# Kernel tuning notes

Hardware: AMD Instinct MI355X
Metric: run time of the kernel (lower is better)

## Reference

```python
import jax, jax.numpy as jnp
import numpy as np

BLOCK_SIZE = 16
NVFP4_LEVELS = np.array([0.0, 0.5, 1.0, 1.5, 2.0, 3.0, 4.0, 6.0], dtype=np.float32)


def quantize_to_nvfp4(x, block_size=BLOCK_SIZE):
    """NVFP4 fake-quant: per-16-element block, scale = amax/6, round |x| to nearest level."""
    levels = jnp.asarray(NVFP4_LEVELS, dtype=x.dtype)
    orig_shape = x.shape
    xf = x.reshape(-1, block_size)                                   # [nblk, 16]
    amax = jnp.clip(jnp.max(jnp.abs(xf), axis=-1, keepdims=True), 1e-12)
    scale = amax / 6.0                                               # [nblk, 1]
    x_norm = jnp.abs(xf) / scale                                     # in [0, 6]
    idx = jnp.argmin(jnp.abs(x_norm[..., None] - levels), axis=-1)   # nearest level (first on ties, like torch)
    x_q = jnp.sign(xf) * levels[idx] * scale
    return x_q.reshape(orig_shape)


def _magnitude_mask_2_4(w):
    # keep 2 largest-|.| of every group of 4 along in_features (row-wise 2:4)
    out_f, in_f = w.shape
    a = jnp.abs(w).reshape(out_f, in_f // 4, 4)
    thr = jnp.sort(a, axis=-1)[..., 2:3]          # 2nd-largest magnitude in group
    mask = (a >= thr).reshape(out_f, in_f)
    return mask.astype(w.dtype)


def setup_inputs() -> dict:
    key = jax.random.key(0)
    k_x, k_w, k_s, k_a, k_b, k_bias = jax.random.split(key, 6)
    B, S, IN_F, OUT_F, RANK = 2, 2048, 4096, 4096, 32
    x = jax.random.normal(k_x, (B, S, IN_F), dtype=jnp.float32)
    smooth_scale = jax.random.uniform(k_s, (IN_F,), dtype=jnp.float32, minval=0.5, maxval=2.0)
    # realistic calibrated weight: 2:4 magnitude-sparse then NVFP4 fake-quantized
    w = jax.random.normal(k_w, (OUT_F, IN_F), dtype=jnp.float32) * 0.02
    w_sparse = w * _magnitude_mask_2_4(w)
    w_quantized = quantize_to_nvfp4(w_sparse)
    lora_a = jax.random.normal(k_a, (RANK, IN_F), dtype=jnp.float32) * 0.02
    lora_b = jax.random.normal(k_b, (OUT_F, RANK), dtype=jnp.float32) * 0.02
    bias = jax.random.normal(k_bias, (OUT_F,), dtype=jnp.float32)
    return {"x": x, "smooth_scale": smooth_scale, "w_quantized": w_quantized,
            "lora_a": lora_a, "lora_b": lora_b, "bias": bias}


def reference(x, smooth_scale, w_quantized, lora_a, lora_b, bias):
    # x: [B, S, IN], smooth_scale: [IN], w_quantized: [OUT, IN]
    x_smoothed = x * smooth_scale                                    # SmoothQuant activation scaling
    x_q = quantize_to_nvfp4(x_smoothed, BLOCK_SIZE)                  # block fake-quant of activations
    base_out = jnp.einsum('bsi,oi->bso', x_q, w_quantized)           # 2:4-sparse quantized matmul
    svd_out = jnp.einsum('bsr,or->bso',
                         jnp.einsum('bsi,ri->bsr', x_smoothed, lora_a), lora_b)  # low-rank correction
    return base_out + svd_out + bias
```

## Files before the change

kernel.cpp:

```cpp
#include <hip/hip_runtime.h>
#include <hip/hip_bf16.h>
#include <stdint.h>

typedef __attribute__((ext_vector_type(8)))  __bf16 bf16x8;
typedef __attribute__((ext_vector_type(4)))  float  f32x4;
typedef __attribute__((ext_vector_type(16))) float  f32x16;

#define KP 4160

__device__ inline void async_copy16(const void* g, void* l) {
  __builtin_amdgcn_global_load_lds((const __attribute__((address_space(1))) void*)g,
                                   (__attribute__((address_space(3))) void*)l, 16, 0, 0);
}

__global__ __launch_bounds__(256) void fused_quant_lora_kernel(
    const float* __restrict__ x, const float* __restrict__ ss,
    const float* __restrict__ la, __bf16* __restrict__ Ab,
    float* __restrict__ Tp) {
  __shared__ float red[4][16][32];
  int tid  = threadIdx.x;
  int m0   = blockIdx.x << 4;
  int by   = blockIdx.y;

  {
    int row = m0 + (tid >> 4);
    int cb0 = tid & 15;
#pragma unroll
    for (int i = 0; i < 4; i++) {
      int col = (by << 10) + ((cb0 + (i << 4)) << 4);
      const float4* xp = (const float4*)(x + ((size_t)row << 12) + col);
      const float4* sp = (const float4*)(ss + col);
      float xs[16];
#pragma unroll
      for (int j = 0; j < 4; j++) {
        float4 xv = xp[j]; float4 sv = sp[j];
        xs[4*j+0] = xv.x * sv.x; xs[4*j+1] = xv.y * sv.y;
        xs[4*j+2] = xv.z * sv.z; xs[4*j+3] = xv.w * sv.w;
      }
      float amax = 0.f;
#pragma unroll
      for (int j = 0; j < 16; j++) amax = fmaxf(amax, fabsf(xs[j]));
      amax = fmaxf(amax, 1e-12f);
      float scale = amax / 6.0f;
      bf16x8 o0, o1;
#pragma unroll
      for (int j = 0; j < 16; j++) {
        float a  = fabsf(xs[j]);
        float xn = a / scale;
        float bestd = xn;
        float lvl   = 0.f;
        const float L[7] = {0.5f, 1.f, 1.5f, 2.f, 3.f, 4.f, 6.f};
#pragma unroll
        for (int l = 0; l < 7; l++) {
          float d = fabsf(xn - L[l]);
          if (d < bestd) { bestd = d; lvl = L[l]; }
        }
        float mag = lvl * scale;
        float q = (xs[j] > 0.f) ? mag : ((xs[j] < 0.f) ? -mag : 0.f);
        if (j < 8) o0[j] = (__bf16)q; else o1[j-8] = (__bf16)q;
      }
      __bf16* dst = Ab + (size_t)row * KP + col;
      *(bf16x8*)dst = o0;
      *(bf16x8*)(dst + 8) = o1;
    }
  }

  {
    int wave = tid >> 6, lane = tid & 63;
    int lrow = lane & 15, kg = lane >> 4;
    int kbase = (by << 10) + (wave << 8);
    f32x4 acc0 = {0.f,0.f,0.f,0.f}, acc1 = {0.f,0.f,0.f,0.f};
    const float* xrow = x + ((size_t)(m0 + lrow) << 12);
    const float* a0   = la + ((size_t)lrow << 12);
    const float* a1   = a0 + (16 << 12);
#pragma unroll
    for (int k0 = 0; k0 < 256; k0 += 32) {
      int kk = kbase + k0 + (kg << 3);
      float xv[8], sv[8], v0[8], v1[8];
      *(float4*)&xv[0] = *(const float4*)(xrow + kk);
      *(float4*)&xv[4] = *(const float4*)(xrow + kk + 4);
      *(float4*)&sv[0] = *(const float4*)(ss + kk);
      *(float4*)&sv[4] = *(const float4*)(ss + kk + 4);
      *(float4*)&v0[0] = *(const float4*)(a0 + kk);
      *(float4*)&v0[4] = *(const float4*)(a0 + kk + 4);
      *(float4*)&v1[0] = *(const float4*)(a1 + kk);
      *(float4*)&v1[4] = *(const float4*)(a1 + kk + 4);
      bf16x8 af, b0, b1;
#pragma unroll
      for (int j = 0; j < 8; j++) {
        af[j] = (__bf16)(xv[j] * sv[j]);
        b0[j] = (__bf16)v0[j];
        b1[j] = (__bf16)v1[j];
      }
      acc0 = __builtin_amdgcn_mfma_f32_16x16x32_bf16(af, b0, acc0, 0, 0, 0);
      acc1 = __builtin_amdgcn_mfma_f32_16x16x32_bf16(af, b1, acc1, 0, 0, 0);
    }
#pragma unroll
    for (int r = 0; r < 4; r++) {
      red[wave][kg*4 + r][lrow]      = acc0[r];
      red[wave][kg*4 + r][16 + lrow] = acc1[r];
    }
    __syncthreads();
    for (int o = tid; o < 512; o += 256) {
      int rr = o >> 5, cc = o & 31;
      float s = red[0][rr][cc] + red[1][rr][cc] + red[2][rr][cc] + red[3][rr][cc];
      Tp[((size_t)by * 4096 + m0 + rr) * 32 + cc] = s;
    }
  }
}

__global__ __launch_bounds__(256) void wconv_fix_kernel(const float* __restrict__ w,
                                                        const float* __restrict__ lb,
                                                        const float* __restrict__ Tp,
                                                        __bf16* __restrict__ Bb,
                                                        __bf16* __restrict__ Ab) {
  int b = blockIdx.x;
  if (b < 8320) {
    int id  = b * 256 + threadIdx.x;
    int row = id / 520;
    int g   = id - row * 520;
    bf16x8 v;
    if (g < 512) {
      const float4* wp = (const float4*)(w + ((size_t)row << 12) + (g << 3));
      float4 a = wp[0], bb = wp[1];
      v[0]=(__bf16)a.x;  v[1]=(__bf16)a.y;  v[2]=(__bf16)a.z;  v[3]=(__bf16)a.w;
      v[4]=(__bf16)bb.x; v[5]=(__bf16)bb.y; v[6]=(__bf16)bb.z; v[7]=(__bf16)bb.w;
    } else if (g < 516) {
      const float* p = lb + (size_t)row * 32 + ((g - 512) << 3);
#pragma unroll
      for (int j = 0; j < 8; j++) v[j] = (__bf16)p[j];
    } else {
#pragma unroll
      for (int j = 0; j < 8; j++) v[j] = (__bf16)0.f;
    }
    *(bf16x8*)(Bb + (size_t)row * KP + ((size_t)g << 3)) = v;
  } else {
    int id  = (b - 8320) * 256 + threadIdx.x;
    int row = id >> 5, cc = id & 31;
    float s = 0.f;
#pragma unroll
    for (int kc = 0; kc < 4; kc++)
      s += Tp[((size_t)kc * 4096 + row) * 32 + cc];
    __bf16* dst = Ab + (size_t)row * KP + 4096;
    dst[cc]      = (__bf16)s;
    dst[32 + cc] = (__bf16)0.f;
  }
}

__global__ __launch_bounds__(256) void gemm_kernel(const __bf16* __restrict__ A,
                                                   const __bf16* __restrict__ B,
                                                   const float* __restrict__ bias,
                                                   float* __restrict__ C) {
  __shared__ __bf16 As[128 * 64];
  __shared__ __bf16 Bs[128 * 64];
  int tid  = threadIdx.x;
  int wave = tid >> 6, lane = tid & 63;
  int bm = blockIdx.x >> 5, bn = blockIdx.x & 31;
  size_t m0 = (size_t)bm << 7, n0 = (size_t)bn << 7;
  int wm = wave >> 1, wn = wave & 1;
  int ln31 = lane & 31, kgrp = lane >> 5;
  int srow = lane >> 3;
  int sk   = ((lane & 7) ^ srow) << 3;
  int swz  = (ln31 & 7) << 4;
  f32x16 acc[2][2];
#pragma unroll
  for (int r = 0; r < 2; r++)
#pragma unroll
    for (int c = 0; c < 2; c++)
#pragma unroll
      for (int q = 0; q < 16; q++) acc[r][c][q] = 0.f;

  for (int k = 0; k < KP; k += 64) {
#pragma unroll
    for (int i = 0; i < 4; i++) {
      int chunk = (wave << 2) + i;
      int row   = (chunk << 3) + srow;
      async_copy16(A + (m0 + row) * (size_t)KP + k + sk, (void*)(As + chunk * 512));
      async_copy16(B + (n0 + row) * (size_t)KP + k + sk, (void*)(Bs + chunk * 512));
    }
    __syncthreads();
#pragma unroll
    for (int t = 0; t < 4; t++) {
      int kx = ((t << 5) + (kgrp << 4)) ^ swz;
      bf16x8 af[2], bfr[2];
#pragma unroll
      for (int h = 0; h < 2; h++) {
        int arow = (wm << 6) + (h << 5) + ln31;
        af[h]  = *(const bf16x8*)((const char*)As + arow * 128 + kx);
        int brow = (wn << 6) + (h << 5) + ln31;
        bfr[h] = *(const bf16x8*)((const char*)Bs + brow * 128 + kx);
      }
#pragma unroll
      for (int r = 0; r < 2; r++)
#pragma unroll
        for (int c = 0; c < 2; c++)
          acc[r][c] = __builtin_amdgcn_mfma_f32_32x32x16_bf16(af[r], bfr[c], acc[r][c], 0, 0, 0);
    }
    __syncthreads();
  }
#pragma unroll
  for (int c = 0; c < 2; c++) {
    int col = (int)n0 + (wn << 6) + (c << 5) + ln31;
    float bv = bias[col];
#pragma unroll
    for (int r = 0; r < 2; r++) {
      size_t rowb = m0 + (wm << 6) + (r << 5) + (kgrp << 2);
#pragma unroll
      for (int q = 0; q < 16; q++) {
        size_t row = rowb + (q & 3) + ((q >> 2) << 3);
        C[row * 4096 + col] = acc[r][c][q] + bv;
      }
    }
  }
}

extern "C" void kernel_launch(void* const* d_in, const int* in_sizes, int n_in,
                              void* d_out, int out_size, void* d_ws, size_t ws_size,
                              hipStream_t stream) {
  const float* x    = (const float*)d_in[0];
  const float* ss   = (const float*)d_in[1];
  const float* w    = (const float*)d_in[2];
  const float* la   = (const float*)d_in[3];
  const float* lb   = (const float*)d_in[4];
  const float* bias = (const float*)d_in[5];
  float* out = (float*)d_out;

  __bf16* Ab = (__bf16*)d_ws;
  __bf16* Bb = Ab + (size_t)4096 * KP;
  float* Tp = out;

  fused_quant_lora_kernel<<<dim3(256, 4), 256, 0, stream>>>(x, ss, la, Ab, Tp);
  wconv_fix_kernel<<<8832, 256, 0, stream>>>(w, lb, Tp, Bb, Ab);
  gemm_kernel<<<1024, 256, 0, stream>>>(Ab, Bb, bias, out);
}
```

Baseline: 348.3 us.

## Rewrite GEMM as 256x256 tiled, double-buffered, barrier-scheduled 8-wave kernel

Replaces the 128x128, single-buffered GEMM with a 256x256 tile per 512-thread block. It double-buffers 128 KB of dynamic LDS, interleaves async global-to-LDS copies with MFMA phases, and uses s_setprio and explicit vmcnt waits to overlap loads with compute. K padding grows to 4224 so K is a multiple of 128 for the two-stage pipeline, with extra zero fill. A block-index swizzle improves L2 locality. This targets the low arithmetic intensity and exposed load latency of the old GEMM, at the cost of heavy register and LDS use and only 256 blocks.

```diff
diff --git a/kernel.cpp b/kernel.cpp
--- a/kernel.cpp
+++ b/kernel.cpp
@@ -4,9 +4,8 @@
 
 typedef __attribute__((ext_vector_type(8)))  __bf16 bf16x8;
 typedef __attribute__((ext_vector_type(4)))  float  f32x4;
-typedef __attribute__((ext_vector_type(16))) float  f32x16;
-
-#define KP 4160
+
+#define KP 4224
 
 __device__ inline void async_copy16(const void* g, void* l) {
   __builtin_amdgcn_global_load_lds((const __attribute__((address_space(1))) void*)g,
@@ -115,10 +114,10 @@
                                                         __bf16* __restrict__ Bb,
                                                         __bf16* __restrict__ Ab) {
   int b = blockIdx.x;
-  if (b < 8320) {
+  if (b < 8448) {
     int id  = b * 256 + threadIdx.x;
-    int row = id / 520;
-    int g   = id - row * 520;
+    int row = id / 528;
+    int g   = id - row * 528;
     bf16x8 v;
     if (g < 512) {
       const float4* wp = (const float4*)(w + ((size_t)row << 12) + (g << 3));
@@ -135,7 +134,7 @@
     }
     *(bf16x8*)(Bb + (size_t)row * KP + ((size_t)g << 3)) = v;
   } else {
-    int id  = (b - 8320) * 256 + threadIdx.x;
+    int id  = (b - 8448) * 256 + threadIdx.x;
     int row = id >> 5, cc = id & 31;
     float s = 0.f;
 #pragma unroll
@@ -144,72 +143,129 @@
     __bf16* dst = Ab + (size_t)row * KP + 4096;
     dst[cc]      = (__bf16)s;
     dst[32 + cc] = (__bf16)0.f;
-  }
-}
-
-__global__ __launch_bounds__(256) void gemm_kernel(const __bf16* __restrict__ A,
-                                                   const __bf16* __restrict__ B,
-                                                   const float* __restrict__ bias,
-                                                   float* __restrict__ C) {
-  __shared__ __bf16 As[128 * 64];
-  __shared__ __bf16 Bs[128 * 64];
-  int tid  = threadIdx.x;
-  int wave = tid >> 6, lane = tid & 63;
-  int bm = blockIdx.x >> 5, bn = blockIdx.x & 31;
-  size_t m0 = (size_t)bm << 7, n0 = (size_t)bn << 7;
-  int wm = wave >> 1, wn = wave & 1;
-  int ln31 = lane & 31, kgrp = lane >> 5;
-  int srow = lane >> 3;
-  int sk   = ((lane & 7) ^ srow) << 3;
-  int swz  = (ln31 & 7) << 4;
-  f32x16 acc[2][2];
-#pragma unroll
-  for (int r = 0; r < 2; r++)
-#pragma unroll
-    for (int c = 0; c < 2; c++)
-#pragma unroll
-      for (int q = 0; q < 16; q++) acc[r][c][q] = 0.f;
-
-  for (int k = 0; k < KP; k += 64) {
-#pragma unroll
-    for (int i = 0; i < 4; i++) {
-      int chunk = (wave << 2) + i;
-      int row   = (chunk << 3) + srow;
-      async_copy16(A + (m0 + row) * (size_t)KP + k + sk, (void*)(As + chunk * 512));
-      async_copy16(B + (n0 + row) * (size_t)KP + k + sk, (void*)(Bs + chunk * 512));
-    }
-    __syncthreads();
-#pragma unroll
-    for (int t = 0; t < 4; t++) {
-      int kx = ((t << 5) + (kgrp << 4)) ^ swz;
-      bf16x8 af[2], bfr[2];
-#pragma unroll
-      for (int h = 0; h < 2; h++) {
-        int arow = (wm << 6) + (h << 5) + ln31;
-        af[h]  = *(const bf16x8*)((const char*)As + arow * 128 + kx);
-        int brow = (wn << 6) + (h << 5) + ln31;
-        bfr[h] = *(const bf16x8*)((const char*)Bs + brow * 128 + kx);
-      }
-#pragma unroll
-      for (int r = 0; r < 2; r++)
-#pragma unroll
-        for (int c = 0; c < 2; c++)
-          acc[r][c] = __builtin_amdgcn_mfma_f32_32x32x16_bf16(af[r], bfr[c], acc[r][c], 0, 0, 0);
-    }
-    __syncthreads();
-  }
-#pragma unroll
-  for (int c = 0; c < 2; c++) {
-    int col = (int)n0 + (wn << 6) + (c << 5) + ln31;
-    float bv = bias[col];
-#pragma unroll
-    for (int r = 0; r < 2; r++) {
-      size_t rowb = m0 + (wm << 6) + (r << 5) + (kgrp << 2);
-#pragma unroll
-      for (int q = 0; q < 16; q++) {
-        size_t row = rowb + (q & 3) + ((q >> 2) << 3);
-        C[row * 4096 + col] = acc[r][c][q] + bv;
-      }
+    dst[64 + cc] = (__bf16)0.f;
+    dst[96 + cc] = (__bf16)0.f;
+  }
+}
+
+#define GBAR() __builtin_amdgcn_s_barrier()
+#define PRI1() __builtin_amdgcn_s_setprio(1)
+#define PRI0() __builtin_amdgcn_s_setprio(0)
+#define WVM(n) asm volatile("s_waitcnt vmcnt(" #n ")" ::: "memory")
+
+#define STG(srcb, dstb, bb, h, t) do {                                         \
+    const __bf16* _s = (srcb) + (size_t)(h) * (128 * (size_t)KP)               \
+                              + ((size_t)(t) << 6);                            \
+    char* _d = (dstb) + ((bb) << 15) + ((h) << 14);                            \
+    async_copy16(_s, _d);                                                      \
+    async_copy16(_s + 32, _d + 1024);                                          \
+  } while (0)
+
+#define RDA(p, MFB) do { _Pragma("unroll")                                     \
+  for (int u = 0; u < 8; u++)                                                  \
+    Afr[u] = *(const bf16x8*)((p) + ((((MFB)*2) + u) << 10)); } while (0)
+
+#define RDB(p, NFB) do { _Pragma("unroll")                                     \
+  for (int u = 0; u < 4; u++)                                                  \
+    Bfr[(NFB)*2 + u] = *(const bf16x8*)((p) + ((((NFB)*2) + u) << 10)); } while (0)
+
+#define MM(MFB, NFB) do {                                                      \
+  _Pragma("unroll") for (int mf = 0; mf < 4; mf++)                             \
+  _Pragma("unroll") for (int nf = 0; nf < 2; nf++)                             \
+  _Pragma("unroll") for (int ks = 0; ks < 2; ks++)                             \
+    acc[(MFB)+mf][(NFB)+nf] = __builtin_amdgcn_mfma_f32_16x16x32_bf16(         \
+        Afr[mf*2+ks], Bfr[((NFB)+nf)*2+ks], acc[(MFB)+mf][(NFB)+nf], 0, 0, 0); \
+  } while (0)
+
+__global__ __launch_bounds__(512, 2) void gemm_kernel(const __bf16* __restrict__ A,
+                                                      const __bf16* __restrict__ B,
+                                                      const float* __restrict__ bias,
+                                                      float* __restrict__ C) {
+  extern __shared__ char lds[];
+  const int tid  = threadIdx.x;
+  const int w    = tid >> 6, lane = tid & 63;
+  const int ln15 = lane & 15, kg = lane >> 4;
+  const int wm   = w >> 2, wn = w & 3;
+  const int bid  = blockIdx.x;
+  const int sbid = ((bid & 7) << 5) | (bid >> 3);
+  const int bm   = sbid >> 4, bn = sbid & 15;
+  const size_t m0 = (size_t)bm << 8, n0 = (size_t)bn << 8;
+
+  const int rr = (w << 4) + (lane >> 2);
+  const int kk = ((lane & 3) ^ (((lane >> 5) & 1) << 1)) << 3;
+  const __bf16* aS = A + (m0 + rr) * (size_t)KP + kk;
+  const __bf16* bS = B + (n0 + rr) * (size_t)KP + kk;
+  char* dA = lds + (w << 11);
+  char* dB = lds + 65536 + (w << 11);
+
+  int inner = (ln15 << 6) + (kg << 4);
+  inner ^= (ln15 & 8) << 2;
+  const char* pA0 = lds + (wm << 14) + inner;
+  const char* pA1 = pA0 + 32768;
+  const char* pB0 = lds + 65536 + (wn << 13) + inner;
+  const char* pB1 = pB0 + 32768;
+
+  bf16x8 Afr[8], Bfr[8];
+  f32x4 acc[8][4];
+#pragma unroll
+  for (int i = 0; i < 8; i++)
+#pragma unroll
+    for (int j = 0; j < 4; j++) acc[i][j] = (f32x4){0.f, 0.f, 0.f, 0.f};
+
+  STG(bS, dB, 0, 0, 0); STG(bS, dB, 0, 1, 0);
+  STG(aS, dA, 0, 0, 0); STG(aS, dA, 0, 1, 0);
+  STG(bS, dB, 1, 0, 1); STG(bS, dB, 1, 1, 1);
+  WVM(4);
+  GBAR();
+
+#pragma unroll 1
+  for (int i = 0; i < 32; i++) {
+    const int t1 = 2*i + 1, t2 = 2*i + 2, t3 = 2*i + 3;
+    RDA(pA0, 0); RDB(pB0, 0); STG(aS, dA, 1, 0, t1);
+    GBAR(); PRI1(); MM(0, 0); PRI0(); GBAR();
+    RDB(pB0, 2); STG(aS, dA, 1, 1, t1);
+    GBAR(); PRI1(); MM(0, 2); PRI0(); GBAR();
+    RDA(pA0, 4); STG(bS, dB, 0, 0, t2);
+    GBAR(); PRI1(); MM(4, 0); PRI0(); GBAR();
+    STG(bS, dB, 0, 1, t2);
+    GBAR(); PRI1(); MM(4, 2); PRI0(); WVM(4); GBAR();
+    RDA(pA1, 0); RDB(pB1, 0); STG(aS, dA, 0, 0, t2);
+    GBAR(); PRI1(); MM(0, 0); PRI0(); GBAR();
+    RDB(pB1, 2); STG(aS, dA, 0, 1, t2);
+    GBAR(); PRI1(); MM(0, 2); PRI0(); GBAR();
+    RDA(pA1, 4); STG(bS, dB, 1, 0, t3);
+    GBAR(); PRI1(); MM(4, 0); PRI0(); GBAR();
+    STG(bS, dB, 1, 1, t3);
+    GBAR(); PRI1(); MM(4, 2); PRI0(); WVM(4); GBAR();
+  }
+
+  RDA(pA0, 0); RDB(pB0, 0); STG(aS, dA, 1, 0, 65);
+  GBAR(); PRI1(); MM(0, 0); PRI0(); GBAR();
+  RDB(pB0, 2); STG(aS, dA, 1, 1, 65);
+  GBAR(); PRI1(); MM(0, 2); PRI0(); GBAR();
+  RDA(pA0, 4);
+  GBAR(); PRI1(); MM(4, 0); PRI0(); GBAR();
+  GBAR(); PRI1(); MM(4, 2); PRI0(); WVM(0); GBAR();
+  RDA(pA1, 0); RDB(pB1, 0);
+  GBAR(); PRI1(); MM(0, 0); PRI0(); GBAR();
+  RDB(pB1, 2);
+  GBAR(); PRI1(); MM(0, 2); PRI0(); GBAR();
+  RDA(pA1, 4);
+  GBAR(); PRI1(); MM(4, 0); PRI0(); GBAR();
+  GBAR(); PRI1(); MM(4, 2); PRI0(); GBAR();
+
+  const int    colb = (int)n0 + (wn << 6) + ln15;
+  const size_t rowb = m0 + ((size_t)wm << 7) + (kg << 2);
+#pragma unroll
+  for (int nf = 0; nf < 4; nf++) {
+    const int col = colb + (nf << 4);
+    const float bv = bias[col];
+#pragma unroll
+    for (int mf = 0; mf < 8; mf++) {
+      const size_t r0 = rowb + ((size_t)mf << 4);
+#pragma unroll
+      for (int q = 0; q < 4; q++)
+        C[(r0 + q) * 4096 + col] = acc[mf][nf][q] + bv;
     }
   }
 }
@@ -229,7 +285,14 @@
   __bf16* Bb = Ab + (size_t)4096 * KP;
   float* Tp = out;
 
+  static bool s_attr = false;
+  if (!s_attr) {
+    hipFuncSetAttribute((const void*)gemm_kernel,
+                        hipFuncAttributeMaxDynamicSharedMemorySize, 131072);
+    s_attr = true;
+  }
+
   fused_quant_lora_kernel<<<dim3(256, 4), 256, 0, stream>>>(x, ss, la, Ab, Tp);
-  wconv_fix_kernel<<<8832, 256, 0, stream>>>(w, lb, Tp, Bb, Ab);
-  gemm_kernel<<<1024, 256, 0, stream>>>(Ab, Bb, bias, out);
-}
+  wconv_fix_kernel<<<8960, 256, 0, stream>>>(w, lb, Tp, Bb, Ab);
+  gemm_kernel<<<256, 512, 131072, stream>>>(Ab, Bb, bias, out);
+}
```

Measured after the change: 311.0 us. 1.12x faster.
